# Kernel optimization log

Measured on AMD Instinct MI355X. Metric: run time of the kernel, lower is better.

Reference implementation:

```python
import jax, jax.numpy as jnp
import numpy as np

USER = 100000
ITEM = 50000
N = USER + ITEM          # total nodes in bipartite graph
LAT = 64                 # args.latdim
TXT = 768                # args.text_feat_dim
E = 2400000              # nnz per sparse adjacency
GNN_LAYERS = 2           # args.gnn_layer
RIS_LAMBDA = 0.2         # args.ris_adj_lambda


def setup_inputs() -> dict:
    key = jax.random.key(0)
    ks = jax.random.split(key, 11)
    return {
        "uEmbeds": jax.random.normal(ks[0], (USER, LAT), jnp.float32) * 0.1,
        "iEmbeds": jax.random.normal(ks[1], (ITEM, LAT), jnp.float32) * 0.1,
        "text_embedding": jax.random.normal(ks[2], (ITEM, TXT), jnp.float32),
        "W_text": jax.random.normal(ks[3], (TXT, LAT), jnp.float32) * (1.0 / np.sqrt(TXT)),
        "b_text": jnp.zeros((LAT,), jnp.float32),
        "adj_vals": jax.random.uniform(ks[4], (E,), jnp.float32) / 16.0,
        "t_vals": jax.random.uniform(ks[5], (E,), jnp.float32) / 16.0,
        "adj_rows": jax.random.randint(ks[6], (E,), 0, N, jnp.int32),
        "adj_cols": jax.random.randint(ks[7], (E,), 0, N, jnp.int32),
        "t_rows": jax.random.randint(ks[8], (E,), 0, N, jnp.int32),
        "t_cols": jax.random.randint(ks[9], (E,), 0, N, jnp.int32),
    }


def _spmm(rows, cols, vals, x, n):
    # out[r] = sum_{e: rows[e]==r} vals[e] * x[cols[e]]  (torch.spmm on COO)
    return jax.ops.segment_sum(vals[:, None] * x[cols], rows, num_segments=n)


def _l2_normalize(x, eps=1e-12):
    # F.normalize(x, p=2, dim=1)
    nrm = jnp.sqrt(jnp.sum(x * x, axis=1, keepdims=True))
    return x / jnp.maximum(nrm, eps)


def reference(uEmbeds, iEmbeds, text_embedding, W_text, b_text,
              adj_vals, t_vals, adj_rows, adj_cols, t_rows, t_cols):
    # trans == 1: Linear projection of text features
    text_feats = text_embedding @ W_text + b_text                      # [ITEM, LAT]

    # self-propagation through text adjacency
    embeds_ta = _spmm(t_rows, t_cols, t_vals,
                      jnp.concatenate([uEmbeds, iEmbeds], axis=0), N)  # [N, LAT]

    # first hop: users + normalized text feats
    e1 = _spmm(adj_rows, adj_cols, adj_vals,
               jnp.concatenate([uEmbeds, _l2_normalize(text_feats)], axis=0), N)

    # second hop: aggregated users + raw item embeds
    e2 = _spmm(adj_rows, adj_cols, adj_vals,
               jnp.concatenate([e1[:USER], iEmbeds], axis=0), N)

    embeds = e1 + e2 + RIS_LAMBDA * embeds_ta

    # stacked GCN layers, sum of all layer outputs (incl. layer 0)
    total = embeds
    cur = embeds
    for _ in range(GNN_LAYERS):
        cur = _spmm(adj_rows, adj_cols, adj_vals, cur, N)
        total = total + cur

    return total[:USER], total[USER:]
```

## Files before the change

### kernel.cpp

```cpp
#include <hip/hip_runtime.h>
#include <hip/hip_fp16.h>

#define USER  100000
#define ITEM  50000
#define NNODE 150000
#define LAT   64
#define TXT   768
#define RP    150016
#define NBUCK 8
#define BROWS (NNODE / NBUCK)
#define SCHUNK 4096
#define CAP   64
#define GEMMB 782

typedef unsigned long long u64;

__device__ __forceinline__ void store4(float* p, float4 v) { *(float4*)p = v; }
__device__ __forceinline__ void store4(__half* p, float4 v)
{
    __half2* d = (__half2*)p;
    d[0] = __floats2half2_rn(v.x, v.y);
    d[1] = __floats2half2_rn(v.z, v.w);
}
__device__ __forceinline__ float4 load_x4(const float* x, int l)
{
    return *(const float4*)(x + 4 * l);
}
__device__ __forceinline__ float4 load_x4(const __half* x, int l)
{
    float2 raw = *(const float2*)(x + 4 * l);
    __half2 h0 = *reinterpret_cast<const __half2*>(&raw.x);
    __half2 h1 = *reinterpret_cast<const __half2*>(&raw.y);
    float2 f0 = __half22float2(h0);
    float2 f1 = __half22float2(h1);
    return make_float4(f0.x, f0.y, f1.x, f1.y);
}

template<typename TFT>
__device__ __forceinline__ void gemm_body(
    float (*As)[68], float (*Bs)[64],
    const float* __restrict__ text, const float* __restrict__ W,
    const float* __restrict__ b, TFT* __restrict__ tf,
    int nitems, int blk)
{
    const int tid = threadIdx.x;
    const int tx  = tid & 15;
    const int ty  = tid >> 4;
    const int row0 = blk * 64;

    float acc[4][4] = {};

    const int lrow = tid >> 3;
    const int lk4  = (tid & 7) * 4;

    for (int k0 = 0; k0 < TXT; k0 += 32) {
#pragma unroll
        for (int half = 0; half < 2; ++half) {
            int r = lrow + half * 32;
            int gr = row0 + r;
            if (gr >= nitems) gr = nitems - 1;
            float4 tv = *(const float4*)(text + (size_t)gr * TXT + k0 + lk4);
            As[lk4 + 0][r] = tv.x;
            As[lk4 + 1][r] = tv.y;
            As[lk4 + 2][r] = tv.z;
            As[lk4 + 3][r] = tv.w;
        }
        const float4* wf = (const float4*)(W + (size_t)k0 * LAT);
        ((float4*)Bs)[tid]       = wf[tid];
        ((float4*)Bs)[tid + 256] = wf[tid + 256];
        __syncthreads();

#pragma unroll
        for (int k = 0; k < 32; ++k) {
            float4 a4 = *(const float4*)&As[k][ty * 4];
            float4 b4 = *(const float4*)&Bs[k][tx * 4];
            float av[4] = {a4.x, a4.y, a4.z, a4.w};
            float bv[4] = {b4.x, b4.y, b4.z, b4.w};
#pragma unroll
            for (int i = 0; i < 4; ++i)
#pragma unroll
                for (int j = 0; j < 4; ++j)
                    acc[i][j] = fmaf(av[i], bv[j], acc[i][j]);
        }
        __syncthreads();
    }

    float4 b4 = *(const float4*)(b + tx * 4);
    float bv[4] = {b4.x, b4.y, b4.z, b4.w};
#pragma unroll
    for (int i = 0; i < 4; ++i) {
        float v[4];
        float ss = 0.f;
#pragma unroll
        for (int j = 0; j < 4; ++j) {
            v[j] = acc[i][j] + bv[j];
            ss = fmaf(v[j], v[j], ss);
        }
        ss += __shfl_xor(ss, 1);
        ss += __shfl_xor(ss, 2);
        ss += __shfl_xor(ss, 4);
        ss += __shfl_xor(ss, 8);
        float inv = 1.0f / fmaxf(sqrtf(ss), 1e-12f);
        int gr = row0 + ty * 4 + i;
        if (gr < nitems)
            store4(tf + (size_t)gr * LAT + tx * 4,
                   make_float4(v[0] * inv, v[1] * inv, v[2] * inv, v[3] * inv));
    }
}

__device__ __forceinline__ void scatter_body(
    const int* __restrict__ rows, const int* __restrict__ cols,
    const float* __restrict__ vals, int* __restrict__ fil,
    u64* __restrict__ epk, int n, int bucket, int chunk)
{
    const int lo = bucket * BROWS;
    const int hi = lo + BROWS;
    const int base = chunk * SCHUNK + threadIdx.x;

    int  r[16];
    bool m[16];
    u64  pk[16];
    int  pos[16];

#pragma unroll
    for (int i = 0; i < 16; ++i) {
        int e = base + i * 256;
        bool inb = e < n;
        int rr = inb ? rows[e] : -1;
        r[i] = rr;
        m[i] = inb && (rr >= lo) && (rr < hi);
    }
#pragma unroll
    for (int i = 0; i < 16; ++i) {
        int e = base + i * 256;
        if (m[i])
            pk[i] = ((u64)__float_as_uint(vals[e]) << 32) | (unsigned)cols[e];
    }
#pragma unroll
    for (int i = 0; i < 16; ++i)
        if (m[i]) pos[i] = atomicAdd(&fil[r[i]], 1);
#pragma unroll
    for (int i = 0; i < 16; ++i)
        if (m[i] && pos[i] < CAP)
            epk[((size_t)r[i] << 6) + pos[i]] = pk[i];
}

__device__ __forceinline__ void cvt_body(
    const float* __restrict__ u, const float* __restrict__ it,
    __half* __restrict__ u16, __half* __restrict__ it16,
    int slot, int nslots)
{
    const long NG  = (long)NNODE * LAT / 8;
    const long UG  = (long)USER * LAT / 8;
    const long stride = (long)nslots * 256;
    for (long g = (long)slot * 256 + threadIdx.x; g < NG; g += stride) {
        const float* s; __half* d; long off;
        if (g < UG) { s = u;  d = u16;  off = g * 8; }
        else        { s = it; d = it16; off = (g - UG) * 8; }
        const float4* s4 = (const float4*)(s + off);
        float4 a = s4[0], c = s4[1];
        __half2* d2 = (__half2*)(d + off);
        d2[0] = __floats2half2_rn(a.x, a.y);
        d2[1] = __floats2half2_rn(a.z, a.w);
        d2[2] = __floats2half2_rn(c.x, c.y);
        d2[3] = __floats2half2_rn(c.z, c.w);
    }
}

template<typename TFT>
__global__ __launch_bounds__(256) void mega1_kernel(
    const float* __restrict__ text, const float* __restrict__ W,
    const float* __restrict__ b, TFT* __restrict__ tf, int nitems,
    const int* __restrict__ arows, const int* __restrict__ acols,
    const float* __restrict__ avals, int* __restrict__ filA, u64* __restrict__ epkA,
    const int* __restrict__ trows, const int* __restrict__ tcols,
    const float* __restrict__ tvals, int* __restrict__ filT, u64* __restrict__ epkT,
    int nedges, int nchunk, int nscat,
    const float* __restrict__ u, const float* __restrict__ it,
    __half* __restrict__ u16, __half* __restrict__ it16, int ncvt)
{
    __shared__ float As[32][68];
    __shared__ float Bs[32][64];

    const int bid = blockIdx.x;
    const int gi  = bid / 72;
    const int pos = bid % 72;

    if (pos < 64) {
        const int so = gi * 64 + pos;
        if (so >= nscat) return;
        const int bucket = so & 7;
        const int cm     = so >> 3;
        if (cm < nchunk)
            scatter_body(arows, acols, avals, filA, epkA, nedges, bucket, cm);
        else
            scatter_body(trows, tcols, tvals, filT, epkT, nedges, bucket, cm - nchunk);
    } else {
        const int go = gi * 8 + (pos - 64);
        if (go < GEMMB)
            gemm_body<TFT>(As, Bs, text, W, b, tf, nitems, go);
        else if (u16 && go - GEMMB < ncvt)
            cvt_body(u, it, u16, it16, go - GEMMB, ncvt);
    }
}

__global__ __launch_bounds__(256) void gemm_norm_kernel(
    const float* __restrict__ text, const float* __restrict__ W,
    const float* __restrict__ b, float* __restrict__ tf, int nitems)
{
    __shared__ float As[32][68];
    __shared__ float Bs[32][64];
    gemm_body<float>(As, Bs, text, W, b, tf, nitems, blockIdx.x);
}

template<typename XT>
__device__ __forceinline__ void spmm_row(
    int r, int lane, const int* __restrict__ cnt, const u64* __restrict__ epk,
    const XT* __restrict__ xu, const XT* __restrict__ xi,
    float scale, const float* __restrict__ add1, const float* __restrict__ add2,
    float* __restrict__ out32, __half* __restrict__ out16)
{
    const int g = lane >> 4;
    const int l = lane & 15;

    const u64* rowp = epk + ((size_t)r << 6);
    const int deg = min(cnt[r], CAP);

    float4 acc = {0.f, 0.f, 0.f, 0.f};

    u64 pk[4];
#pragma unroll
    for (int i = 0; i < 4; ++i) pk[i] = rowp[g + i * 4];
#pragma unroll
    for (int i = 0; i < 4; ++i) {
        int ee = g + i * 4;
        if (ee < deg) {
            int   c = (int)(unsigned)(pk[i] & 0xffffffffu);
            float v = __uint_as_float((unsigned)(pk[i] >> 32));
            const XT* x = (c < USER) ? (xu + (size_t)c * LAT)
                                     : (xi + (size_t)(c - USER) * LAT);
            float4 xv = load_x4(x, l);
            acc.x = fmaf(v, xv.x, acc.x);
            acc.y = fmaf(v, xv.y, acc.y);
            acc.z = fmaf(v, xv.z, acc.z);
            acc.w = fmaf(v, xv.w, acc.w);
        }
    }

    if (deg > 16) {
        u64 pk2[4];
#pragma unroll
        for (int i = 0; i < 4; ++i) pk2[i] = rowp[16 + g + i * 4];
#pragma unroll
        for (int i = 0; i < 4; ++i) {
            int ee = 16 + g + i * 4;
            if (ee < deg) {
                int   c = (int)(unsigned)(pk2[i] & 0xffffffffu);
                float v = __uint_as_float((unsigned)(pk2[i] >> 32));
                const XT* x = (c < USER) ? (xu + (size_t)c * LAT)
                                         : (xi + (size_t)(c - USER) * LAT);
                float4 xv = load_x4(x, l);
                acc.x = fmaf(v, xv.x, acc.x);
                acc.y = fmaf(v, xv.y, acc.y);
                acc.z = fmaf(v, xv.z, acc.z);
                acc.w = fmaf(v, xv.w, acc.w);
            }
        }
        for (int ee = 32 + g; ee < deg; ee += 4) {
            u64 p = rowp[ee];
            int   c = (int)(unsigned)(p & 0xffffffffu);
            float v = __uint_as_float((unsigned)(p >> 32));
            const XT* x = (c < USER) ? (xu + (size_t)c * LAT)
                                     : (xi + (size_t)(c - USER) * LAT);
            float4 xv = load_x4(x, l);
            acc.x = fmaf(v, xv.x, acc.x);
            acc.y = fmaf(v, xv.y, acc.y);
            acc.z = fmaf(v, xv.z, acc.z);
            acc.w = fmaf(v, xv.w, acc.w);
        }
    }

#pragma unroll
    for (int off = 16; off <= 32; off <<= 1) {
        acc.x += __shfl_xor(acc.x, off);
        acc.y += __shfl_xor(acc.y, off);
        acc.z += __shfl_xor(acc.z, off);
        acc.w += __shfl_xor(acc.w, off);
    }
    if (g == 0) {
        size_t idx = (size_t)r * LAT + 4 * l;
        float4 res = {scale * acc.x, scale * acc.y, scale * acc.z, scale * acc.w};
        if (add1) {
            float4 a = *(const float4*)(add1 + idx);
            res.x += a.x; res.y += a.y; res.z += a.z; res.w += a.w;
        }
        if (add2) {
            float4 a = *(const float4*)(add2 + idx);
            res.x += a.x; res.y += a.y; res.z += a.z; res.w += a.w;
        }
        *(float4*)(out32 + idx) = res;
        if (out16) store4(out16 + idx, res);
    }
}

template<typename XT>
__global__ __launch_bounds__(256) void spmm_kernel(
    const int* __restrict__ cnt, const u64* __restrict__ epk,
    const XT* __restrict__ xu, const XT* __restrict__ xi,
    float scale, const float* __restrict__ add1, const float* __restrict__ add2,
    float* __restrict__ out32, __half* __restrict__ out16, int n)
{
    int r = blockIdx.x * 4 + (threadIdx.x >> 6);
    if (r >= n) return;
    spmm_row<XT>(r, threadIdx.x & 63, cnt, epk, xu, xi, scale,
                 add1, add2, out32, out16);
}

template<typename XT>
__global__ __launch_bounds__(256) void spmm_pair_kernel(
    const int* __restrict__ cnt0, const u64* __restrict__ epk0,
    const XT* __restrict__ xu0, const XT* __restrict__ xi0,
    float s0, float* __restrict__ out0, __half* __restrict__ o16_0,
    const int* __restrict__ cnt1, const u64* __restrict__ epk1,
    const XT* __restrict__ xu1, const XT* __restrict__ xi1,
    float s1, float* __restrict__ out1, __half* __restrict__ o16_1, int n)
{
    int m  = blockIdx.x & 1;
    int r  = (blockIdx.x >> 1) * 4 + (threadIdx.x >> 6);
    if (r >= n) return;
    int lane = threadIdx.x & 63;
    if (m == 0)
        spmm_row<XT>(r, lane, cnt0, epk0, xu0, xi0, s0, nullptr, nullptr,
                     out0, o16_0);
    else
        spmm_row<XT>(r, lane, cnt1, epk1, xu1, xi1, s1, nullptr, nullptr,
                     out1, o16_1);
}

__global__ __launch_bounds__(256) void spmm_atomic_kernel(
    const int* __restrict__ rows, const int* __restrict__ cols,
    const float* __restrict__ vals, float scale,
    const float* __restrict__ xu, const float* __restrict__ xi,
    float* __restrict__ out, int nedges)
{
    int e = blockIdx.x * 4 + (threadIdx.x >> 6);
    if (e >= nedges) return;
    int lane = threadIdx.x & 63;
    int r = rows[e];
    int c = cols[e];
    float v = vals[e] * scale;
    const float* x = (c < USER) ? (xu + (size_t)c * LAT)
                                : (xi + (size_t)(c - USER) * LAT);
    atomicAdd(&out[(size_t)r * LAT + lane], v * x[lane]);
}

__global__ __launch_bounds__(256) void combine_kernel(
    float* __restrict__ A, const float* __restrict__ B,
    float* __restrict__ out, int n4)
{
    int i = blockIdx.x * blockDim.x + threadIdx.x;
    if (i >= n4) return;
    float4 a = ((const float4*)A)[i];
    float4 b = ((const float4*)B)[i];
    a.x += b.x; a.y += b.y; a.z += b.z; a.w += b.w;
    ((float4*)A)[i]   = a;
    ((float4*)out)[i] = a;
}

__global__ __launch_bounds__(256) void add_kernel(
    float* __restrict__ out, const float* __restrict__ src, int n4)
{
    int i = blockIdx.x * blockDim.x + threadIdx.x;
    if (i >= n4) return;
    float4 o = ((const float4*)out)[i];
    float4 s = ((const float4*)src)[i];
    o.x += s.x; o.y += s.y; o.z += s.z; o.w += s.w;
    ((float4*)out)[i] = o;
}

extern "C" void kernel_launch(void* const* d_in, const int* in_sizes, int n_in,
                              void* d_out, int out_size, void* d_ws, size_t ws_size,
                              hipStream_t stream)
{
    const float* u        = (const float*)d_in[0];
    const float* it       = (const float*)d_in[1];
    const float* text     = (const float*)d_in[2];
    const float* W        = (const float*)d_in[3];
    const float* b        = (const float*)d_in[4];
    const float* adj_vals = (const float*)d_in[5];
    const float* t_vals   = (const float*)d_in[6];
    const int*   adj_rows = (const int*)d_in[7];
    const int*   adj_cols = (const int*)d_in[8];
    const int*   t_rows   = (const int*)d_in[9];
    const int*   t_cols   = (const int*)d_in[10];
    const int E = in_sizes[5];

    float* out = (float*)d_out;

    const int sblk   = (NNODE + 3) / 4;
    const int nchunk = (E + SCHUNK - 1) / SCHUNK;
    const int nscat  = 2 * nchunk * NBUCK;
    const int ngrp   = (nscat + 63) / 64;
    const int ncvt   = ngrp * 8 - GEMMB;
    const int n4     = NNODE * LAT / 4;
    const int cblk   = (n4 + 255) / 256;

    char* p = (char*)d_ws;
    size_t used = 0;
    auto carve = [&](size_t bytes) {
        char* q = p + used;
        used += (bytes + 255) & ~(size_t)255;
        return q;
    };

    used = 0;
    float*  A    = (float*) carve((size_t)NNODE * LAT * 4);
    float*  B    = (float*) carve((size_t)NNODE * LAT * 4);
    int*    filA = (int*)   carve((size_t)RP * 4);
    int*    filT = (int*)   carve((size_t)RP * 4);
    u64*    epkA = (u64*)   carve((size_t)E ? (size_t)NNODE * CAP * 8 : 0);
    u64*    epkT = (u64*)   carve((size_t)NNODE * CAP * 8);
    __half* tf16 = (__half*)carve((size_t)ITEM * LAT * 2);
    __half* u16  = (__half*)carve((size_t)NNODE * LAT * 2);
    __half* it16 = u16 + (size_t)USER * LAT;
    __half* B16  = (__half*)carve((size_t)NNODE * LAT * 2);
    __half* A16  = (__half*)epkT;

    if (used <= ws_size && ncvt > 0) {
        hipMemsetAsync(filA, 0, (size_t)RP * 4 * 2, stream);
        mega1_kernel<__half><<<ngrp * 72, 256, 0, stream>>>(
            text, W, b, tf16, ITEM,
            adj_rows, adj_cols, adj_vals, filA, epkA,
            t_rows, t_cols, t_vals, filT, epkT, E, nchunk, nscat,
            u, it, u16, it16, ncvt);

        spmm_pair_kernel<__half><<<sblk * 2, 256, 0, stream>>>(
            filT, epkT, u16, it16, 0.2f, A, nullptr,
            filA, epkA, u16, tf16, 1.0f, B, B16, NNODE);

        spmm_kernel<__half><<<sblk, 256, 0, stream>>>(
            filA, epkA, B16, it16, 1.0f, A, B, A, A16, NNODE);
        spmm_kernel<__half><<<sblk, 256, 0, stream>>>(
            filA, epkA, A16, A16 + (size_t)USER * LAT, 1.0f,
            nullptr, nullptr, B, B16, NNODE);
        spmm_kernel<__half><<<sblk, 256, 0, stream>>>(
            filA, epkA, B16, B16 + (size_t)USER * LAT, 1.0f,
            A, B, out, nullptr, NNODE);
        return;
    }

    used = 0;
    float* A2    = (float*)carve((size_t)NNODE * LAT * 4);
    float* B2    = (float*)carve((size_t)NNODE * LAT * 4);
    float* tf2   = (float*)carve((size_t)ITEM * LAT * 4);
    int*   filA2 = (int*)  carve((size_t)RP * 4);
    int*   filT2 = (int*)  carve((size_t)RP * 4);
    u64*   epkA2 = (u64*)  carve((size_t)NNODE * CAP * 8);
    u64*   epkT2 = (u64*)  carve((size_t)NNODE * CAP * 8);

    if (used <= ws_size) {
        hipMemsetAsync(filA2, 0, (size_t)RP * 4 * 2, stream);
        mega1_kernel<float><<<ngrp * 72, 256, 0, stream>>>(
            text, W, b, tf2, ITEM,
            adj_rows, adj_cols, adj_vals, filA2, epkA2,
            t_rows, t_cols, t_vals, filT2, epkT2, E, nchunk, nscat,
            u, it, nullptr, nullptr, 0);

        spmm_pair_kernel<float><<<sblk * 2, 256, 0, stream>>>(
            filT2, epkT2, u, it, 0.2f, A2, nullptr,
            filA2, epkA2, u, tf2, 1.0f, B2, nullptr, NNODE);

        spmm_kernel<float><<<sblk, 256, 0, stream>>>(
            filA2, epkA2, B2, it, 1.0f, A2, B2, A2, nullptr, NNODE);
        spmm_kernel<float><<<sblk, 256, 0, stream>>>(
            filA2, epkA2, A2, A2 + (size_t)USER * LAT, 1.0f,
            nullptr, nullptr, B2, nullptr, NNODE);
        spmm_kernel<float><<<sblk, 256, 0, stream>>>(
            filA2, epkA2, B2, B2 + (size_t)USER * LAT, 1.0f,
            A2, B2, out, nullptr, NNODE);
        return;
    }

    used = 0;
    float* A3  = (float*)carve((size_t)NNODE * LAT * 4);
    float* B3  = (float*)carve((size_t)NNODE * LAT * 4);
    float* tf3 = (float*)carve((size_t)ITEM * LAT * 4);
    const size_t nbuf = (size_t)NNODE * LAT * 4;
    const int ablk = (E + 3) / 4;
    const int gblk = (ITEM + 63) / 64;
    gemm_norm_kernel<<<gblk, 256, 0, stream>>>(text, W, b, tf3, ITEM);
    hipMemsetAsync(A3, 0, nbuf, stream);
    hipMemsetAsync(B3, 0, nbuf, stream);
    spmm_atomic_kernel<<<ablk, 256, 0, stream>>>(t_rows, t_cols, t_vals, 0.2f,
                                                 u, it, A3, E);
    spmm_atomic_kernel<<<ablk, 256, 0, stream>>>(adj_rows, adj_cols, adj_vals, 1.0f,
                                                 u, tf3, B3, E);
    spmm_atomic_kernel<<<ablk, 256, 0, stream>>>(adj_rows, adj_cols, adj_vals, 1.0f,
                                                 B3, it, A3, E);
    combine_kernel<<<cblk, 256, 0, stream>>>(A3, B3, out, n4);
    hipMemsetAsync(B3, 0, nbuf, stream);
    spmm_atomic_kernel<<<ablk, 256, 0, stream>>>(adj_rows, adj_cols, adj_vals, 1.0f,
                                                 A3, A3 + (size_t)USER * LAT, B3, E);
    add_kernel<<<cblk, 256, 0, stream>>>(out, B3, n4);
    hipMemsetAsync(A3, 0, nbuf, stream);
    spmm_atomic_kernel<<<ablk, 256, 0, stream>>>(adj_rows, adj_cols, adj_vals, 1.0f,
                                                 B3, B3 + (size_t)USER * LAT, A3, E);
    add_kernel<<<cblk, 256, 0, stream>>>(out, A3, n4);
}
```

Measured before the change: 647.9 us.

## Split preprocessing kernel to overlap text-adjacency SpMM with adjacency bucketing

The single mega preprocessing kernel is split in two. The first builds the text-adjacency buckets, runs the GEMM and does the fp16 conversion. The second builds the main-adjacency buckets while other blocks run the text-adjacency SpMM, so gather work overlaps the scatter work. The first-hop SpMM becomes its own kernel, and the intermediate hop now writes only an fp16 copy, which the final pass reads back through a new half-precision addend input. This saves fp32 stores and loads of one buffer, at the cost of adding fp16 rounding to that term and of a different launch and occupancy mix.

```diff
diff --git a/kernel.cpp b/kernel.cpp
--- a/kernel.cpp
+++ b/kernel.cpp
@@ -22,18 +22,22 @@
     d[0] = __floats2half2_rn(v.x, v.y);
     d[1] = __floats2half2_rn(v.z, v.w);
 }
-__device__ __forceinline__ float4 load_x4(const float* x, int l)
-{
-    return *(const float4*)(x + 4 * l);
-}
-__device__ __forceinline__ float4 load_x4(const __half* x, int l)
-{
-    float2 raw = *(const float2*)(x + 4 * l);
+__device__ __forceinline__ float4 loadh4(const __half* p)
+{
+    float2 raw = *(const float2*)p;
     __half2 h0 = *reinterpret_cast<const __half2*>(&raw.x);
     __half2 h1 = *reinterpret_cast<const __half2*>(&raw.y);
     float2 f0 = __half22float2(h0);
     float2 f1 = __half22float2(h1);
     return make_float4(f0.x, f0.y, f1.x, f1.y);
+}
+__device__ __forceinline__ float4 load_x4(const float* x, int l)
+{
+    return *(const float4*)(x + 4 * l);
+}
+__device__ __forceinline__ float4 load_x4(const __half* x, int l)
+{
+    return loadh4(x + 4 * l);
 }
 
 template<typename TFT>
@@ -167,6 +171,155 @@
     }
 }
 
+template<typename XT>
+__device__ __forceinline__ void spmm_row(
+    int r, int lane, const int* __restrict__ cnt, const u64* __restrict__ epk,
+    const XT* __restrict__ xu, const XT* __restrict__ xi,
+    float scale, const float* __restrict__ add1, const float* __restrict__ add2,
+    const __half* __restrict__ add2h,
+    float* __restrict__ out32, __half* __restrict__ out16)
+{
+    const int g = lane >> 4;
+    const int l = lane & 15;
+
+    const u64* rowp = epk + ((size_t)r << 6);
+    const int deg = min(cnt[r], CAP);
+
+    float4 acc = {0.f, 0.f, 0.f, 0.f};
+
+    u64 pk[4];
+#pragma unroll
+    for (int i = 0; i < 4; ++i) pk[i] = rowp[g + i * 4];
+#pragma unroll
+    for (int i = 0; i < 4; ++i) {
+        int ee = g + i * 4;
+        if (ee < deg) {
+            int   c = (int)(unsigned)(pk[i] & 0xffffffffu);
+            float v = __uint_as_float((unsigned)(pk[i] >> 32));
+            const XT* x = (c < USER) ? (xu + (size_t)c * LAT)
+                                     : (xi + (size_t)(c - USER) * LAT);
+            float4 xv = load_x4(x, l);
+            acc.x = fmaf(v, xv.x, acc.x);
+            acc.y = fmaf(v, xv.y, acc.y);
+            acc.z = fmaf(v, xv.z, acc.z);
+            acc.w = fmaf(v, xv.w, acc.w);
+        }
+    }
+
+    if (deg > 16) {
+        u64 pk2[4];
+#pragma unroll
+        for (int i = 0; i < 4; ++i) pk2[i] = rowp[16 + g + i * 4];
+#pragma unroll
+        for (int i = 0; i < 4; ++i) {
+            int ee = 16 + g + i * 4;
+            if (ee < deg) {
+                int   c = (int)(unsigned)(pk2[i] & 0xffffffffu);
+                float v = __uint_as_float((unsigned)(pk2[i] >> 32));
+                const XT* x = (c < USER) ? (xu + (size_t)c * LAT)
+                                         : (xi + (size_t)(c - USER) * LAT);
+                float4 xv = load_x4(x, l);
+                acc.x = fmaf(v, xv.x, acc.x);
+                acc.y = fmaf(v, xv.y, acc.y);
+                acc.z = fmaf(v, xv.z, acc.z);
+                acc.w = fmaf(v, xv.w, acc.w);
+            }
+        }
+        for (int ee = 32 + g; ee < deg; ee += 4) {
+            u64 p = rowp[ee];
+            int   c = (int)(unsigned)(p & 0xffffffffu);
+            float v = __uint_as_float((unsigned)(p >> 32));
+            const XT* x = (c < USER) ? (xu + (size_t)c * LAT)
+                                     : (xi + (size_t)(c - USER) * LAT);
+            float4 xv = load_x4(x, l);
+            acc.x = fmaf(v, xv.x, acc.x);
+            acc.y = fmaf(v, xv.y, acc.y);
+            acc.z = fmaf(v, xv.z, acc.z);
+            acc.w = fmaf(v, xv.w, acc.w);
+        }
+    }
+
+#pragma unroll
+    for (int off = 16; off <= 32; off <<= 1) {
+        acc.x += __shfl_xor(acc.x, off);
+        acc.y += __shfl_xor(acc.y, off);
+        acc.z += __shfl_xor(acc.z, off);
+        acc.w += __shfl_xor(acc.w, off);
+    }
+    if (g == 0) {
+        size_t idx = (size_t)r * LAT + 4 * l;
+        float4 res = {scale * acc.x, scale * acc.y, scale * acc.z, scale * acc.w};
+        if (add1) {
+            float4 a = *(const float4*)(add1 + idx);
+            res.x += a.x; res.y += a.y; res.z += a.z; res.w += a.w;
+        }
+        if (add2) {
+            float4 a = *(const float4*)(add2 + idx);
+            res.x += a.x; res.y += a.y; res.z += a.z; res.w += a.w;
+        }
+        if (add2h) {
+            float4 a = loadh4(add2h + idx);
+            res.x += a.x; res.y += a.y; res.z += a.z; res.w += a.w;
+        }
+        if (out32) *(float4*)(out32 + idx) = res;
+        if (out16) store4(out16 + idx, res);
+    }
+}
+
+__global__ __launch_bounds__(256) void mega1a_kernel(
+    const float* __restrict__ text, const float* __restrict__ W,
+    const float* __restrict__ b, __half* __restrict__ tf, int nitems,
+    const int* __restrict__ trows, const int* __restrict__ tcols,
+    const float* __restrict__ tvals, int* __restrict__ filT, u64* __restrict__ epkT,
+    int nedges, int nchunk,
+    const float* __restrict__ u, const float* __restrict__ it,
+    __half* __restrict__ u16, __half* __restrict__ it16, int ncvt)
+{
+    __shared__ float As[32][68];
+    __shared__ float Bs[32][64];
+
+    const int bid = blockIdx.x;
+    const int gi  = bid >> 4;
+    const int pos = bid & 15;
+
+    if (pos < 8) {
+        const int so = gi * 8 + pos;
+        if ((so >> 3) < nchunk)
+            scatter_body(trows, tcols, tvals, filT, epkT, nedges, so & 7, so >> 3);
+    } else {
+        const int go = gi * 8 + (pos - 8);
+        if (go < GEMMB)
+            gemm_body<__half>(As, Bs, text, W, b, tf, nitems, go);
+        else if (go - GEMMB < ncvt)
+            cvt_body(u, it, u16, it16, go - GEMMB, ncvt);
+    }
+}
+
+__global__ __launch_bounds__(256) void mega1b_kernel(
+    const int* __restrict__ arows, const int* __restrict__ acols,
+    const float* __restrict__ avals, int* __restrict__ filA, u64* __restrict__ epkA,
+    int nedges, int nchunk,
+    const int* __restrict__ filT, const u64* __restrict__ epkT,
+    const __half* __restrict__ u16, const __half* __restrict__ it16,
+    float* __restrict__ A)
+{
+    const int bid = blockIdx.x;
+    const int gi  = bid / 72;
+    const int pos = bid % 72;
+
+    if (pos < 8) {
+        const int so = gi * 8 + pos;
+        if ((so >> 3) < nchunk)
+            scatter_body(arows, acols, avals, filA, epkA, nedges, so & 7, so >> 3);
+    } else {
+        const int so2 = gi * 64 + (pos - 8);
+        int r = so2 * 4 + (threadIdx.x >> 6);
+        if (r < NNODE)
+            spmm_row<__half>(r, threadIdx.x & 63, filT, epkT, u16, it16, 0.2f,
+                             nullptr, nullptr, nullptr, A, nullptr);
+    }
+}
+
 template<typename TFT>
 __global__ __launch_bounds__(256) void mega1_kernel(
     const float* __restrict__ text, const float* __restrict__ W,
@@ -175,9 +328,7 @@
     const float* __restrict__ avals, int* __restrict__ filA, u64* __restrict__ epkA,
     const int* __restrict__ trows, const int* __restrict__ tcols,
     const float* __restrict__ tvals, int* __restrict__ filT, u64* __restrict__ epkT,
-    int nedges, int nchunk, int nscat,
-    const float* __restrict__ u, const float* __restrict__ it,
-    __half* __restrict__ u16, __half* __restrict__ it16, int ncvt)
+    int nedges, int nchunk, int nscat)
 {
     __shared__ float As[32][68];
     __shared__ float Bs[32][64];
@@ -199,8 +350,6 @@
         const int go = gi * 8 + (pos - 64);
         if (go < GEMMB)
             gemm_body<TFT>(As, Bs, text, W, b, tf, nitems, go);
-        else if (u16 && go - GEMMB < ncvt)
-            cvt_body(u, it, u16, it16, go - GEMMB, ncvt);
     }
 }
 
@@ -211,96 +360,6 @@
     __shared__ float As[32][68];
     __shared__ float Bs[32][64];
     gemm_body<float>(As, Bs, text, W, b, tf, nitems, blockIdx.x);
-}
-
-template<typename XT>
-__device__ __forceinline__ void spmm_row(
-    int r, int lane, const int* __restrict__ cnt, const u64* __restrict__ epk,
-    const XT* __restrict__ xu, const XT* __restrict__ xi,
-    float scale, const float* __restrict__ add1, const float* __restrict__ add2,
-    float* __restrict__ out32, __half* __restrict__ out16)
-{
-    const int g = lane >> 4;
-    const int l = lane & 15;
-
-    const u64* rowp = epk + ((size_t)r << 6);
-    const int deg = min(cnt[r], CAP);
-
-    float4 acc = {0.f, 0.f, 0.f, 0.f};
-
-    u64 pk[4];
-#pragma unroll
-    for (int i = 0; i < 4; ++i) pk[i] = rowp[g + i * 4];
-#pragma unroll
-    for (int i = 0; i < 4; ++i) {
-        int ee = g + i * 4;
-        if (ee < deg) {
-            int   c = (int)(unsigned)(pk[i] & 0xffffffffu);
-            float v = __uint_as_float((unsigned)(pk[i] >> 32));
-            const XT* x = (c < USER) ? (xu + (size_t)c * LAT)
-                                     : (xi + (size_t)(c - USER) * LAT);
-            float4 xv = load_x4(x, l);
-            acc.x = fmaf(v, xv.x, acc.x);
-            acc.y = fmaf(v, xv.y, acc.y);
-            acc.z = fmaf(v, xv.z, acc.z);
-            acc.w = fmaf(v, xv.w, acc.w);
-        }
-    }
-
-    if (deg > 16) {
-        u64 pk2[4];
-#pragma unroll
-        for (int i = 0; i < 4; ++i) pk2[i] = rowp[16 + g + i * 4];
-#pragma unroll
-        for (int i = 0; i < 4; ++i) {
-            int ee = 16 + g + i * 4;
-            if (ee < deg) {
-                int   c = (int)(unsigned)(pk2[i] & 0xffffffffu);
-                float v = __uint_as_float((unsigned)(pk2[i] >> 32));
-                const XT* x = (c < USER) ? (xu + (size_t)c * LAT)
-                                         : (xi + (size_t)(c - USER) * LAT);
-                float4 xv = load_x4(x, l);
-                acc.x = fmaf(v, xv.x, acc.x);
-                acc.y = fmaf(v, xv.y, acc.y);
-                acc.z = fmaf(v, xv.z, acc.z);
-                acc.w = fmaf(v, xv.w, acc.w);
-            }
-        }
-        for (int ee = 32 + g; ee < deg; ee += 4) {
-            u64 p = rowp[ee];
-            int   c = (int)(unsigned)(p & 0xffffffffu);
-            float v = __uint_as_float((unsigned)(p >> 32));
-            const XT* x = (c < USER) ? (xu + (size_t)c * LAT)
-                                     : (xi + (size_t)(c - USER) * LAT);
-            float4 xv = load_x4(x, l);
-            acc.x = fmaf(v, xv.x, acc.x);
-            acc.y = fmaf(v, xv.y, acc.y);
-            acc.z = fmaf(v, xv.z, acc.z);
-            acc.w = fmaf(v, xv.w, acc.w);
-        }
-    }
-
-#pragma unroll
-    for (int off = 16; off <= 32; off <<= 1) {
-        acc.x += __shfl_xor(acc.x, off);
-        acc.y += __shfl_xor(acc.y, off);
-        acc.z += __shfl_xor(acc.z, off);
-        acc.w += __shfl_xor(acc.w, off);
-    }
-    if (g == 0) {
-        size_t idx = (size_t)r * LAT + 4 * l;
-        float4 res = {scale * acc.x, scale * acc.y, scale * acc.z, scale * acc.w};
-        if (add1) {
-            float4 a = *(const float4*)(add1 + idx);
-            res.x += a.x; res.y += a.y; res.z += a.z; res.w += a.w;
-        }
-        if (add2) {
-            float4 a = *(const float4*)(add2 + idx);
-            res.x += a.x; res.y += a.y; res.z += a.z; res.w += a.w;
-        }
-        *(float4*)(out32 + idx) = res;
-        if (out16) store4(out16 + idx, res);
-    }
 }
 
 template<typename XT>
@@ -308,22 +367,23 @@
     const int* __restrict__ cnt, const u64* __restrict__ epk,
     const XT* __restrict__ xu, const XT* __restrict__ xi,
     float scale, const float* __restrict__ add1, const float* __restrict__ add2,
+    const __half* __restrict__ add2h,
     float* __restrict__ out32, __half* __restrict__ out16, int n)
 {
     int r = blockIdx.x * 4 + (threadIdx.x >> 6);
     if (r >= n) return;
     spmm_row<XT>(r, threadIdx.x & 63, cnt, epk, xu, xi, scale,
-                 add1, add2, out32, out16);
+                 add1, add2, add2h, out32, out16);
 }
 
 template<typename XT>
 __global__ __launch_bounds__(256) void spmm_pair_kernel(
     const int* __restrict__ cnt0, const u64* __restrict__ epk0,
     const XT* __restrict__ xu0, const XT* __restrict__ xi0,
-    float s0, float* __restrict__ out0, __half* __restrict__ o16_0,
+    float s0, float* __restrict__ out0,
     const int* __restrict__ cnt1, const u64* __restrict__ epk1,
     const XT* __restrict__ xu1, const XT* __restrict__ xi1,
-    float s1, float* __restrict__ out1, __half* __restrict__ o16_1, int n)
+    float s1, float* __restrict__ out1, int n)
 {
     int m  = blockIdx.x & 1;
     int r  = (blockIdx.x >> 1) * 4 + (threadIdx.x >> 6);
@@ -331,10 +391,10 @@
     int lane = threadIdx.x & 63;
     if (m == 0)
         spmm_row<XT>(r, lane, cnt0, epk0, xu0, xi0, s0, nullptr, nullptr,
-                     out0, o16_0);
+                     nullptr, out0, nullptr);
     else
         spmm_row<XT>(r, lane, cnt1, epk1, xu1, xi1, s1, nullptr, nullptr,
-                     out1, o16_1);
+                     nullptr, out1, nullptr);
 }
 
 __global__ __launch_bounds__(256) void spmm_atomic_kernel(
@@ -399,9 +459,6 @@
 
     const int sblk   = (NNODE + 3) / 4;
     const int nchunk = (E + SCHUNK - 1) / SCHUNK;
-    const int nscat  = 2 * nchunk * NBUCK;
-    const int ngrp   = (nscat + 63) / 64;
-    const int ncvt   = ngrp * 8 - GEMMB;
     const int n4     = NNODE * LAT / 4;
     const int cblk   = (n4 + 255) / 256;
 
@@ -418,7 +475,7 @@
     float*  B    = (float*) carve((size_t)NNODE * LAT * 4);
     int*    filA = (int*)   carve((size_t)RP * 4);
     int*    filT = (int*)   carve((size_t)RP * 4);
-    u64*    epkA = (u64*)   carve((size_t)E ? (size_t)NNODE * CAP * 8 : 0);
+    u64*    epkA = (u64*)   carve((size_t)NNODE * CAP * 8);
     u64*    epkT = (u64*)   carve((size_t)NNODE * CAP * 8);
     __half* tf16 = (__half*)carve((size_t)ITEM * LAT * 2);
     __half* u16  = (__half*)carve((size_t)NNODE * LAT * 2);
@@ -426,26 +483,34 @@
     __half* B16  = (__half*)carve((size_t)NNODE * LAT * 2);
     __half* A16  = (__half*)epkT;
 
-    if (used <= ws_size && ncvt > 0) {
+    const int ngrpa = max(nchunk, (GEMMB + 8 + 7) / 8);
+    const int ncvt  = ngrpa * 8 - GEMMB;
+    const int ngrpb = max(nchunk, (sblk + 63) / 64);
+
+    if (used <= ws_size) {
         hipMemsetAsync(filA, 0, (size_t)RP * 4 * 2, stream);
-        mega1_kernel<__half><<<ngrp * 72, 256, 0, stream>>>(
+
+        mega1a_kernel<<<ngrpa * 16, 256, 0, stream>>>(
             text, W, b, tf16, ITEM,
-            adj_rows, adj_cols, adj_vals, filA, epkA,
-            t_rows, t_cols, t_vals, filT, epkT, E, nchunk, nscat,
+            t_rows, t_cols, t_vals, filT, epkT, E, nchunk,
             u, it, u16, it16, ncvt);
 
-        spmm_pair_kernel<__half><<<sblk * 2, 256, 0, stream>>>(
-            filT, epkT, u16, it16, 0.2f, A, nullptr,
-            filA, epkA, u16, tf16, 1.0f, B, B16, NNODE);
+        mega1b_kernel<<<ngrpb * 72, 256, 0, stream>>>(
+            adj_rows, adj_cols, adj_vals, filA, epkA, E, nchunk,
+            filT, epkT, u16, it16, A);
 
         spmm_kernel<__half><<<sblk, 256, 0, stream>>>(
-            filA, epkA, B16, it16, 1.0f, A, B, A, A16, NNODE);
+            filA, epkA, u16, tf16, 1.0f, nullptr, nullptr, nullptr,
+            B, B16, NNODE);
+
+        spmm_kernel<__half><<<sblk, 256, 0, stream>>>(
+            filA, epkA, B16, it16, 1.0f, A, B, nullptr, A, A16, NNODE);
         spmm_kernel<__half><<<sblk, 256, 0, stream>>>(
             filA, epkA, A16, A16 + (size_t)USER * LAT, 1.0f,
-            nullptr, nullptr, B, B16, NNODE);
+            nullptr, nullptr, nullptr, nullptr, B16, NNODE);
         spmm_kernel<__half><<<sblk, 256, 0, stream>>>(
             filA, epkA, B16, B16 + (size_t)USER * LAT, 1.0f,
-            A, B, out, nullptr, NNODE);
+            A, nullptr, B16, out, nullptr, NNODE);
         return;
     }
 
@@ -459,25 +524,26 @@
     u64*   epkT2 = (u64*)  carve((size_t)NNODE * CAP * 8);
 
     if (used <= ws_size) {
+        const int nscat = 2 * nchunk * NBUCK;
+        const int ngrp  = (nscat + 63) / 64;
         hipMemsetAsync(filA2, 0, (size_t)RP * 4 * 2, stream);
         mega1_kernel<float><<<ngrp * 72, 256, 0, stream>>>(
             text, W, b, tf2, ITEM,
             adj_rows, adj_cols, adj_vals, filA2, epkA2,
-            t_rows, t_cols, t_vals, filT2, epkT2, E, nchunk, nscat,
-            u, it, nullptr, nullptr, 0);
+            t_rows, t_cols, t_vals, filT2, epkT2, E, nchunk, nscat);
 
         spmm_pair_kernel<float><<<sblk * 2, 256, 0, stream>>>(
-            filT2, epkT2, u, it, 0.2f, A2, nullptr,
-            filA2, epkA2, u, tf2, 1.0f, B2, nullptr, NNODE);
+            filT2, epkT2, u, it, 0.2f, A2,
+            filA2, epkA2, u, tf2, 1.0f, B2, NNODE);
 
         spmm_kernel<float><<<sblk, 256, 0, stream>>>(
-            filA2, epkA2, B2, it, 1.0f, A2, B2, A2, nullptr, NNODE);
+            filA2, epkA2, B2, it, 1.0f, A2, B2, nullptr, A2, nullptr, NNODE);
         spmm_kernel<float><<<sblk, 256, 0, stream>>>(
             filA2, epkA2, A2, A2 + (size_t)USER * LAT, 1.0f,
-            nullptr, nullptr, B2, nullptr, NNODE);
+            nullptr, nullptr, nullptr, B2, nullptr, NNODE);
         spmm_kernel<float><<<sblk, 256, 0, stream>>>(
             filA2, epkA2, B2, B2 + (size_t)USER * LAT, 1.0f,
-            A2, B2, out, nullptr, NNODE);
+            A2, B2, nullptr, out, nullptr, NNODE);
         return;
     }
 
```

New measurement: 727.3 us. 1.12x slower.
